# Optimization experiments

Measured on AMD Instinct MI355X. Metric: run time of the kernel, lower is better.

## Reference

```python
import jax, jax.numpy as jnp
import numpy as np

N_NODES = 100000
N_EDGES = 640000
D = 128
L = 3
NUM_GRAPHS = 128


def setup_inputs() -> dict:
    key = jax.random.key(0)
    ks = jax.random.split(key, 8)
    scale = 1.0 / np.sqrt(D)
    x = jax.random.normal(ks[0], (N_NODES, D), dtype=jnp.float32)
    edge_index = jax.random.randint(ks[1], (2, N_EDGES), 0, N_NODES, dtype=jnp.int64)
    batch = jnp.sort(jax.random.randint(ks[2], (N_NODES,), 0, NUM_GRAPHS, dtype=jnp.int64))
    W1 = jax.random.normal(ks[3], (L, D, D), dtype=jnp.float32) * scale
    b1 = jnp.zeros((L, D), dtype=jnp.float32)
    W2 = jax.random.normal(ks[4], (L, D, D), dtype=jnp.float32) * scale
    b2 = jnp.zeros((L, D), dtype=jnp.float32)
    return {"x": x, "edge_index": edge_index, "batch": batch,
            "W1": W1, "b1": b1, "W2": W2, "b2": b2}


def reference(x, edge_index, batch, W1, b1, W2, b2):
    # GIN forward: per layer z = ReLU(MLP((1+eps)*z + sum_{j in N(i)} z_j)), eps=0
    n = x.shape[0]
    src, dst = edge_index[0], edge_index[1]  # messages flow src -> dst
    z = x
    for l in range(W1.shape[0]):
        agg = jax.ops.segment_sum(z[src], dst, num_segments=n)  # scatter-add aggregation
        h = agg + z                                             # (1+eps)*x_i + sum x_j, eps=0
        h = jnp.maximum(h @ W1[l] + b1[l], 0.0)                 # Linear + ReLU
        z = h @ W2[l] + b2[l]                                   # Linear
        z = jnp.maximum(z, 0.0)                                 # F.relu after conv
    # global mean pool over graph ids (dropout is identity in eval / p=0)
    ones = jnp.ones((n,), dtype=z.dtype)
    counts = jax.ops.segment_sum(ones, batch, num_segments=NUM_GRAPHS)
    sums = jax.ops.segment_sum(z, batch, num_segments=NUM_GRAPHS)
    g = sums / jnp.maximum(counts, 1.0)[:, None]
    return z, g
```

## Files before the change

### kernel.cpp

```cpp
#include <hip/hip_runtime.h>
#include <hip/hip_bf16.h>

#define D 128
#define NG 128

typedef __attribute__((ext_vector_type(8))) short bf16x8;
typedef __attribute__((ext_vector_type(4))) float f32x4;

__device__ inline unsigned short f2bf(float f) {
  union { float f; unsigned u; } c; c.f = f;
  unsigned u = c.u;
  return (unsigned short)((u + 0x7FFFu + ((u >> 16) & 1u)) >> 16);
}
__device__ inline float bf2f(unsigned short b) {
  union { unsigned u; float f; } c; c.u = ((unsigned)b) << 16;
  return c.f;
}

__global__ void prep_w(const float* __restrict__ W1, const float* __restrict__ W2,
                       unsigned short* __restrict__ Wt1, unsigned short* __restrict__ Wt2,
                       int* __restrict__ deg, int N, float* __restrict__ g,
                       const int* __restrict__ batch, int* __restrict__ start) {
  int t = blockIdx.x * 256 + threadIdx.x;
  if (t < N) deg[t] = 0;
  if (t < NG * D) g[t] = 0.f;
  if (t < NG) {
    int lo = 0, hi = N;
    while (lo < hi) {
      int mid = (lo + hi) >> 1;
      if (batch[mid] < t) lo = mid + 1; else hi = mid;
    }
    start[t] = lo;
    if (t == 0) start[NG] = N;
  }
  if (t >= 3 * 128 * 128) return;
  int l = t >> 14, k = (t >> 7) & 127, n = t & 127;
  int o = (l << 14) + (n << 7) + k;
  Wt1[o] = f2bf(W1[t]);
  Wt2[o] = f2bf(W2[t]);
}


__global__ void hist_deg(const int* __restrict__ dst, int* __restrict__ deg, int E) {
  int e = blockIdx.x * 256 + threadIdx.x;
  if (e < E) atomicAdd(deg + dst[e], 1);
}

__global__ __launch_bounds__(256) void scan1(const int* __restrict__ deg,
    int* __restrict__ rowptr, int* __restrict__ bsum, int n) {
  __shared__ int sh[256];
  int tid = threadIdx.x;
  int idx = blockIdx.x * 1024 + tid * 4;
  int v[4], tsum = 0;
#pragma unroll
  for (int j = 0; j < 4; ++j) { v[j] = (idx + j < n) ? deg[idx + j] : 0; tsum += v[j]; }
  sh[tid] = tsum;
  __syncthreads();
  for (int off = 1; off < 256; off <<= 1) {
    int x = (tid >= off) ? sh[tid - off] : 0;
    __syncthreads();
    sh[tid] += x;
    __syncthreads();
  }
  if (tid == 255) bsum[blockIdx.x] = sh[255];
  int run = sh[tid] - tsum;
#pragma unroll
  for (int j = 0; j < 4; ++j) { if (idx + j < n) rowptr[idx + j] = run; run += v[j]; }
}

__global__ __launch_bounds__(128) void scan2(int* __restrict__ bsum, int nb) {
  __shared__ int sh[128];
  int tid = threadIdx.x;
  int v = (tid < nb) ? bsum[tid] : 0;
  sh[tid] = v;
  __syncthreads();
  for (int off = 1; off < 128; off <<= 1) {
    int x = (tid >= off) ? sh[tid - off] : 0;
    __syncthreads();
    sh[tid] += x;
    __syncthreads();
  }
  if (tid < nb) bsum[tid] = sh[tid] - v;
}

__global__ void scan3(int* __restrict__ rowptr, int* __restrict__ pos,
                      const int* __restrict__ bsum, int n, int E) {
  int t = blockIdx.x * 256 + threadIdx.x;
  if (t < n) {
    int v = rowptr[t] + bsum[t >> 10];
    rowptr[t] = v;
    pos[t] = v;
  }
  if (t == 0) rowptr[n] = E;
}

__global__ void edge_scatter(const int* __restrict__ src, const int* __restrict__ dst,
                             int* __restrict__ pos, int* __restrict__ csr_src, int E) {
  int e = blockIdx.x * 256 + threadIdx.x;
  if (e >= E) return;
  int idx = atomicAdd(pos + dst[e], 1);
  csr_src[idx] = src[e];
}


template<bool IN_BF16>
__global__ __launch_bounds__(256) void gather_agg(const void* __restrict__ zin,
    const int* __restrict__ rowptr, const int* __restrict__ csr_src,
    unsigned short* __restrict__ agg, int N) {
  int t = blockIdx.x * 256 + threadIdx.x;
  int node = t >> 3;
  if (node >= N) return;
  int c = (t & 7) * 16;
  const float* zf = (const float*)zin;
  const unsigned short* zb = (const unsigned short*)zin;

  float acc[16];

  if constexpr (IN_BF16) {
    const unsigned short* p = zb + (size_t)node * D + c;
    bf16x8 v0 = *(const bf16x8*)(p);
    bf16x8 v1 = *(const bf16x8*)(p + 8);
#pragma unroll
    for (int j = 0; j < 8; ++j) {
      acc[j]     = bf2f((unsigned short)v0[j]);
      acc[j + 8] = bf2f((unsigned short)v1[j]);
    }
  } else {
    const float* p = zf + (size_t)node * D + c;
    float4 v0 = *(const float4*)(p);
    float4 v1 = *(const float4*)(p + 4);
    float4 v2 = *(const float4*)(p + 8);
    float4 v3 = *(const float4*)(p + 12);
    acc[0]  = v0.x; acc[1]  = v0.y; acc[2]  = v0.z; acc[3]  = v0.w;
    acc[4]  = v1.x; acc[5]  = v1.y; acc[6]  = v1.z; acc[7]  = v1.w;
    acc[8]  = v2.x; acc[9]  = v2.y; acc[10] = v2.z; acc[11] = v2.w;
    acc[12] = v3.x; acc[13] = v3.y; acc[14] = v3.z; acc[15] = v3.w;
  }

  int e  = rowptr[node];
  int e1 = rowptr[node + 1];

  if constexpr (IN_BF16) {
    for (; e + 4 <= e1; e += 4) {
      int s0 = csr_src[e + 0];
      int s1 = csr_src[e + 1];
      int s2 = csr_src[e + 2];
      int s3 = csr_src[e + 3];
      const unsigned short* p0 = zb + (size_t)s0 * D + c;
      const unsigned short* p1 = zb + (size_t)s1 * D + c;
      const unsigned short* p2 = zb + (size_t)s2 * D + c;
      const unsigned short* p3 = zb + (size_t)s3 * D + c;
      bf16x8 a0 = *(const bf16x8*)(p0), a1 = *(const bf16x8*)(p0 + 8);
      bf16x8 b0 = *(const bf16x8*)(p1), b1 = *(const bf16x8*)(p1 + 8);
      bf16x8 c0 = *(const bf16x8*)(p2), c1 = *(const bf16x8*)(p2 + 8);
      bf16x8 d0 = *(const bf16x8*)(p3), d1 = *(const bf16x8*)(p3 + 8);
#pragma unroll
      for (int j = 0; j < 8; ++j) {
        acc[j]     += (bf2f((unsigned short)a0[j]) + bf2f((unsigned short)b0[j]))
                    + (bf2f((unsigned short)c0[j]) + bf2f((unsigned short)d0[j]));
        acc[j + 8] += (bf2f((unsigned short)a1[j]) + bf2f((unsigned short)b1[j]))
                    + (bf2f((unsigned short)c1[j]) + bf2f((unsigned short)d1[j]));
      }
    }
    if (e + 2 <= e1) {
      int s0 = csr_src[e + 0];
      int s1 = csr_src[e + 1];
      const unsigned short* p0 = zb + (size_t)s0 * D + c;
      const unsigned short* p1 = zb + (size_t)s1 * D + c;
      bf16x8 a0 = *(const bf16x8*)(p0), a1 = *(const bf16x8*)(p0 + 8);
      bf16x8 b0 = *(const bf16x8*)(p1), b1 = *(const bf16x8*)(p1 + 8);
#pragma unroll
      for (int j = 0; j < 8; ++j) {
        acc[j]     += bf2f((unsigned short)a0[j]) + bf2f((unsigned short)b0[j]);
        acc[j + 8] += bf2f((unsigned short)a1[j]) + bf2f((unsigned short)b1[j]);
      }
      e += 2;
    }
    if (e < e1) {
      int s0 = csr_src[e];
      const unsigned short* p0 = zb + (size_t)s0 * D + c;
      bf16x8 a0 = *(const bf16x8*)(p0), a1 = *(const bf16x8*)(p0 + 8);
#pragma unroll
      for (int j = 0; j < 8; ++j) {
        acc[j]     += bf2f((unsigned short)a0[j]);
        acc[j + 8] += bf2f((unsigned short)a1[j]);
      }
    }
  } else {
    for (; e + 2 <= e1; e += 2) {
      int s0 = csr_src[e + 0];
      int s1 = csr_src[e + 1];
      const float* p0 = zf + (size_t)s0 * D + c;
      const float* p1 = zf + (size_t)s1 * D + c;
      float4 u0 = *(const float4*)(p0);
      float4 u1 = *(const float4*)(p0 + 4);
      float4 u2 = *(const float4*)(p0 + 8);
      float4 u3 = *(const float4*)(p0 + 12);
      float4 w0 = *(const float4*)(p1);
      float4 w1 = *(const float4*)(p1 + 4);
      float4 w2 = *(const float4*)(p1 + 8);
      float4 w3 = *(const float4*)(p1 + 12);
      acc[0]  += u0.x + w0.x; acc[1]  += u0.y + w0.y;
      acc[2]  += u0.z + w0.z; acc[3]  += u0.w + w0.w;
      acc[4]  += u1.x + w1.x; acc[5]  += u1.y + w1.y;
      acc[6]  += u1.z + w1.z; acc[7]  += u1.w + w1.w;
      acc[8]  += u2.x + w2.x; acc[9]  += u2.y + w2.y;
      acc[10] += u2.z + w2.z; acc[11] += u2.w + w2.w;
      acc[12] += u3.x + w3.x; acc[13] += u3.y + w3.y;
      acc[14] += u3.z + w3.z; acc[15] += u3.w + w3.w;
    }
    if (e < e1) {
      int s0 = csr_src[e];
      const float* p0 = zf + (size_t)s0 * D + c;
      float4 u0 = *(const float4*)(p0);
      float4 u1 = *(const float4*)(p0 + 4);
      float4 u2 = *(const float4*)(p0 + 8);
      float4 u3 = *(const float4*)(p0 + 12);
      acc[0]  += u0.x; acc[1]  += u0.y; acc[2]  += u0.z; acc[3]  += u0.w;
      acc[4]  += u1.x; acc[5]  += u1.y; acc[6]  += u1.z; acc[7]  += u1.w;
      acc[8]  += u2.x; acc[9]  += u2.y; acc[10] += u2.z; acc[11] += u2.w;
      acc[12] += u3.x; acc[13] += u3.y; acc[14] += u3.z; acc[15] += u3.w;
    }
  }

  bf16x8 o0, o1;
#pragma unroll
  for (int j = 0; j < 8; ++j) {
    o0[j] = (short)f2bf(acc[j]);
    o1[j] = (short)f2bf(acc[j + 8]);
  }
  unsigned short* q = agg + (size_t)node * D + c;
  *(bf16x8*)(q)     = o0;
  *(bf16x8*)(q + 8) = o1;
}


template<bool LAST>
__global__ __launch_bounds__(256, 2) void gemm_fused(const unsigned short* __restrict__ A,
    const unsigned short* __restrict__ Wt1, const float* __restrict__ b1v,
    const unsigned short* __restrict__ Wt2, const float* __restrict__ b2v,
    unsigned short* __restrict__ Zb, float* __restrict__ Zf, int M, int nt) {
  __shared__ unsigned short w2s[128][136];
  __shared__ unsigned short hs[4][32][136];
  int tid  = threadIdx.x;
  int lane = tid & 63;
  int wid  = tid >> 6;
  int c16  = lane & 15;
  int kq   = lane >> 4;
  int koff = kq * 8;

  int tile0 = blockIdx.x * 2;
  int tile1 = tile0 + 1;

  bf16x8 aA[2][4], aB[2][4];
#pragma unroll
  for (int h = 0; h < 2; ++h) {
    int rowA = tile0 * 128 + wid * 32 + h * 16 + c16;
    rowA = rowA < M ? rowA : M - 1;
    int rowB = tile1 * 128 + wid * 32 + h * 16 + c16;
    rowB = rowB < M ? rowB : M - 1;
#pragma unroll
    for (int kk = 0; kk < 4; ++kk) {
      aA[h][kk] = *(const bf16x8*)(A + (size_t)rowA * D + kk * 32 + koff);
      aB[h][kk] = *(const bf16x8*)(A + (size_t)rowB * D + kk * 32 + koff);
    }
  }

#pragma unroll
  for (int i = 0; i < 8; ++i) {
    int chunk = i * 256 + tid;
    int row = chunk >> 4, k16 = chunk & 15;
    *(bf16x8*)&w2s[row][k16 * 8] = *(const bf16x8*)(Wt2 + (size_t)row * D + k16 * 8);
  }

  bf16x8 bf1[8][4];
  float  bb1[8], bb2[8];
#pragma unroll
  for (int fc = 0; fc < 8; ++fc) {
    int col = fc * 16 + c16;
    bb1[fc] = b1v[col];
    bb2[fc] = b2v[col];
#pragma unroll
    for (int kk = 0; kk < 4; ++kk)
      bf1[fc][kk] = *(const bf16x8*)(Wt1 + (size_t)col * D + kk * 32 + koff);
  }

  __syncthreads();

  auto TILE = [&](const bf16x8 (&a)[2][4], int tile) {
    int rb = tile * 128 + wid * 32;
#pragma unroll
    for (int fc = 0; fc < 8; ++fc) {
      f32x4 acc0 = {0.f, 0.f, 0.f, 0.f};
      f32x4 acc1 = {0.f, 0.f, 0.f, 0.f};
#pragma unroll
      for (int kk = 0; kk < 4; ++kk) {
        acc0 = __builtin_amdgcn_mfma_f32_16x16x32_bf16(a[0][kk], bf1[fc][kk], acc0, 0, 0, 0);
        acc1 = __builtin_amdgcn_mfma_f32_16x16x32_bf16(a[1][kk], bf1[fc][kk], acc1, 0, 0, 0);
      }
      int col = fc * 16 + c16;
#pragma unroll
      for (int r = 0; r < 4; ++r) {
        hs[wid][kq * 4 + r][col]      = f2bf(fmaxf(acc0[r] + bb1[fc], 0.f));
        hs[wid][kq * 4 + r + 16][col] = f2bf(fmaxf(acc1[r] + bb1[fc], 0.f));
      }
    }
    bf16x8 a2[2][4];
#pragma unroll
    for (int fr = 0; fr < 2; ++fr)
#pragma unroll
      for (int kk = 0; kk < 4; ++kk)
        a2[fr][kk] = *(const bf16x8*)&hs[wid][fr * 16 + c16][kk * 32 + koff];
#pragma unroll
    for (int fc = 0; fc < 8; ++fc) {
      f32x4 acc0 = {0.f, 0.f, 0.f, 0.f};
      f32x4 acc1 = {0.f, 0.f, 0.f, 0.f};
      int col = fc * 16 + c16;
#pragma unroll
      for (int kk = 0; kk < 4; ++kk) {
        bf16x8 b = *(const bf16x8*)&w2s[col][kk * 32 + koff];
        acc0 = __builtin_amdgcn_mfma_f32_16x16x32_bf16(a2[0][kk], b, acc0, 0, 0, 0);
        acc1 = __builtin_amdgcn_mfma_f32_16x16x32_bf16(a2[1][kk], b, acc1, 0, 0, 0);
      }
      if constexpr (LAST) {
#pragma unroll
        for (int r = 0; r < 4; ++r) {
          int row0 = rb + kq * 4 + r;
          if (row0 < M) Zf[(size_t)row0 * D + col] = fmaxf(acc0[r] + bb2[fc], 0.f);
          int row1 = row0 + 16;
          if (row1 < M) Zf[(size_t)row1 * D + col] = fmaxf(acc1[r] + bb2[fc], 0.f);
        }
      } else {
#pragma unroll
        for (int r = 0; r < 4; ++r) {
          hs[wid][kq * 4 + r][col]      = f2bf(fmaxf(acc0[r] + bb2[fc], 0.f));
          hs[wid][kq * 4 + r + 16][col] = f2bf(fmaxf(acc1[r] + bb2[fc], 0.f));
        }
      }
    }
    if constexpr (!LAST) {
#pragma unroll
      for (int i = 0; i < 8; ++i) {
        int rl = i * 4 + kq;
        bf16x8 v = *(const bf16x8*)&hs[wid][rl][c16 * 8];
        int row = rb + rl;
        if (row < M)
          *(bf16x8*)(Zb + (size_t)row * D + c16 * 8) = v;
      }
    }
  };

  TILE(aA, tile0);
  if (tile1 < nt) TILE(aB, tile1);
}


#define PCHUNKS 8
__global__ __launch_bounds__(128) void pool_mean(const float* __restrict__ z,
    const int* __restrict__ start, float* __restrict__ g) {
  int gid   = blockIdx.x >> 3;
  int chunk = blockIdx.x & (PCHUNKS - 1);
  int col = threadIdx.x;
  int s = start[gid], epos = start[gid + 1];
  int len = epos - s;
  if (len <= 0) return;
  int per = (len + PCHUNKS - 1) / PCHUNKS;
  int r0 = s + chunk * per;
  int r1 = min(r0 + per, epos);
  if (r0 >= r1) return;
  float a0 = 0.f, a1 = 0.f, a2 = 0.f, a3 = 0.f;
  int i = r0;
  for (; i + 4 <= r1; i += 4) {
    a0 += z[(size_t)(i + 0) * D + col];
    a1 += z[(size_t)(i + 1) * D + col];
    a2 += z[(size_t)(i + 2) * D + col];
    a3 += z[(size_t)(i + 3) * D + col];
  }
  for (; i < r1; ++i) a0 += z[(size_t)i * D + col];
  atomicAdd(g + (size_t)gid * D + col, (a0 + a1) + (a2 + a3));
}

__global__ void pool_div(float* __restrict__ g, const int* __restrict__ start) {
  int t = blockIdx.x * 256 + threadIdx.x;
  if (t >= NG * D) return;
  int gid = t >> 7;
  int cnt = start[gid + 1] - start[gid];
  g[t] = g[t] / fmaxf((float)cnt, 1.f);
}

extern "C" void kernel_launch(void* const* d_in, const int* in_sizes, int n_in,
                              void* d_out, int out_size, void* d_ws, size_t ws_size,
                              hipStream_t stream) {
  const float* x     = (const float*)d_in[0];
  const int*   ei    = (const int*)d_in[1];
  const int*   batch = (const int*)d_in[2];
  const float* W1    = (const float*)d_in[3];
  const float* b1    = (const float*)d_in[4];
  const float* W2    = (const float*)d_in[5];
  const float* b2    = (const float*)d_in[6];

  const int N = in_sizes[0] / D;
  const int E = in_sizes[1] / 2;
  const int* src = ei;
  const int* dst = ei + E;

  float* zout = (float*)d_out;
  float* g    = zout + (size_t)N * D;

  char* w = (char*)d_ws;
  unsigned short* agg     = (unsigned short*)w;    w += (size_t)N * D * 2;
  unsigned short* zb      = (unsigned short*)w;    w += (size_t)N * D * 2;
  unsigned short* Wt1     = (unsigned short*)w;    w += 3 * 16384 * 2;
  unsigned short* Wt2     = (unsigned short*)w;    w += 3 * 16384 * 2;
  int*            start   = (int*)w;               w += (NG + 4) * 4;
  int*            deg     = (int*)w;               w += (size_t)N * 4;
  int*            rowptr  = (int*)w;               w += (size_t)(N + 4) * 4;
  int*            pos     = (int*)w;               w += (size_t)N * 4;
  int*            bsum    = (int*)w;               w += 128 * 4;
  int*            csr_src = (int*)w;               w += (size_t)E * 4;

  const int nb = (N + 1023) / 1024;

  int prep_threads = (3 * 128 * 128 > N) ? 3 * 128 * 128 : N;
  prep_w<<<(prep_threads + 255) / 256, 256, 0, stream>>>(W1, W2, Wt1, Wt2, deg, N, g,
                                                         batch, start);

  hist_deg<<<(E + 255) / 256, 256, 0, stream>>>(dst, deg, E);
  scan1<<<nb, 256, 0, stream>>>(deg, rowptr, bsum, N);
  scan2<<<1, 128, 0, stream>>>(bsum, nb);
  scan3<<<(N + 255) / 256, 256, 0, stream>>>(rowptr, pos, bsum, N, E);
  edge_scatter<<<(E + 255) / 256, 256, 0, stream>>>(src, dst, pos, csr_src, E);

  const int gather_blocks = (int)(((size_t)N * 8 + 255) / 256);
  const int nt            = (N + 127) / 128;
  const int gemm_blocks   = (nt + 1) / 2;

  gather_agg<false><<<gather_blocks, 256, 0, stream>>>(x, rowptr, csr_src, agg, N);
  gemm_fused<false><<<gemm_blocks, 256, 0, stream>>>(agg, Wt1, b1, Wt2, b2, zb, zout, N, nt);
  gather_agg<true><<<gather_blocks, 256, 0, stream>>>(zb, rowptr, csr_src, agg, N);
  gemm_fused<false><<<gemm_blocks, 256, 0, stream>>>(agg, Wt1 + 16384, b1 + 128,
                                                     Wt2 + 16384, b2 + 128, zb, zout, N, nt);
  gather_agg<true><<<gather_blocks, 256, 0, stream>>>(zb, rowptr, csr_src, agg, N);
  gemm_fused<true><<<gemm_blocks, 256, 0, stream>>>(agg, Wt1 + 32768, b1 + 256,
                                                    Wt2 + 32768, b2 + 256, zb, zout, N, nt);

  pool_mean<<<NG * PCHUNKS, 128, 0, stream>>>(zout, start, g);
  pool_div<<<(NG * D + 255) / 256, 256, 0, stream>>>(g, start);
}
```

Before: 279.4 us.

## Fuse CSR build into one cooperative kernel and fold mean division into pooling

Replaces the five CSR construction kernels (degree histogram, three-stage scan, edge scatter) with a single cooperative kernel of 512 blocks that separates phases with grid-wide syncs. Also folds the mean division into pool_mean by scaling partial sums before the atomic add, which removes pool_div. Gather loads of csr_src and stores of agg now use nontemporal hints. Fewer launches cut launch gaps, but the kernel now assumes N ≤ 512*256 and depends on a cooperative launch with grid syncs.

```diff
diff --git a/kernel.cpp b/kernel.cpp
--- a/kernel.cpp
+++ b/kernel.cpp
@@ -1,8 +1,12 @@
 #include <hip/hip_runtime.h>
 #include <hip/hip_bf16.h>
+#include <hip/hip_cooperative_groups.h>
+
+namespace cg = cooperative_groups;
 
 #define D 128
 #define NG 128
+#define CSR_BLOCKS 512
 
 typedef __attribute__((ext_vector_type(8))) short bf16x8;
 typedef __attribute__((ext_vector_type(4))) float f32x4;
@@ -41,20 +45,23 @@
 }
 
 
-__global__ void hist_deg(const int* __restrict__ dst, int* __restrict__ deg, int E) {
-  int e = blockIdx.x * 256 + threadIdx.x;
-  if (e < E) atomicAdd(deg + dst[e], 1);
-}
-
-__global__ __launch_bounds__(256) void scan1(const int* __restrict__ deg,
-    int* __restrict__ rowptr, int* __restrict__ bsum, int n) {
+__global__ __launch_bounds__(256) void csr_build(
+    const int* __restrict__ src, const int* __restrict__ dst,
+    int* __restrict__ deg, int* __restrict__ rowptr, int* __restrict__ pos,
+    int* __restrict__ bsum, int* __restrict__ csr_src, int N, int E) {
+  cg::grid_group grid = cg::this_grid();
   __shared__ int sh[256];
-  int tid = threadIdx.x;
-  int idx = blockIdx.x * 1024 + tid * 4;
-  int v[4], tsum = 0;
-#pragma unroll
-  for (int j = 0; j < 4; ++j) { v[j] = (idx + j < n) ? deg[idx + j] : 0; tsum += v[j]; }
-  sh[tid] = tsum;
+  int tid  = threadIdx.x;
+  int gtid = blockIdx.x * 256 + tid;
+  const int nth = CSR_BLOCKS * 256;
+
+  for (int e = gtid; e < E; e += nth)
+    atomicAdd(deg + dst[e], 1);
+  __threadfence();
+  grid.sync();
+
+  int v = (gtid < N) ? deg[gtid] : 0;
+  sh[tid] = v;
   __syncthreads();
   for (int off = 1; off < 256; off <<= 1) {
     int x = (tid >= off) ? sh[tid - off] : 0;
@@ -63,43 +70,39 @@
     __syncthreads();
   }
   if (tid == 255) bsum[blockIdx.x] = sh[255];
-  int run = sh[tid] - tsum;
-#pragma unroll
-  for (int j = 0; j < 4; ++j) { if (idx + j < n) rowptr[idx + j] = run; run += v[j]; }
-}
-
-__global__ __launch_bounds__(128) void scan2(int* __restrict__ bsum, int nb) {
-  __shared__ int sh[128];
-  int tid = threadIdx.x;
-  int v = (tid < nb) ? bsum[tid] : 0;
-  sh[tid] = v;
-  __syncthreads();
-  for (int off = 1; off < 128; off <<= 1) {
-    int x = (tid >= off) ? sh[tid - off] : 0;
+  int local_ex = sh[tid] - v;
+  __threadfence();
+  grid.sync();
+
+  if (blockIdx.x == 0) {
+    int a = bsum[tid * 2], b = bsum[tid * 2 + 1];
+    int pairsum = a + b;
+    sh[tid] = pairsum;
     __syncthreads();
-    sh[tid] += x;
-    __syncthreads();
-  }
-  if (tid < nb) bsum[tid] = sh[tid] - v;
-}
-
-__global__ void scan3(int* __restrict__ rowptr, int* __restrict__ pos,
-                      const int* __restrict__ bsum, int n, int E) {
-  int t = blockIdx.x * 256 + threadIdx.x;
-  if (t < n) {
-    int v = rowptr[t] + bsum[t >> 10];
-    rowptr[t] = v;
-    pos[t] = v;
-  }
-  if (t == 0) rowptr[n] = E;
-}
-
-__global__ void edge_scatter(const int* __restrict__ src, const int* __restrict__ dst,
-                             int* __restrict__ pos, int* __restrict__ csr_src, int E) {
-  int e = blockIdx.x * 256 + threadIdx.x;
-  if (e >= E) return;
-  int idx = atomicAdd(pos + dst[e], 1);
-  csr_src[idx] = src[e];
+    for (int off = 1; off < 256; off <<= 1) {
+      int x = (tid >= off) ? sh[tid - off] : 0;
+      __syncthreads();
+      sh[tid] += x;
+      __syncthreads();
+    }
+    int ex = sh[tid] - pairsum;
+    bsum[tid * 2]     = ex;
+    bsum[tid * 2 + 1] = ex + a;
+  }
+  __threadfence();
+  grid.sync();
+
+  if (gtid < N) {
+    int val = local_ex + bsum[blockIdx.x];
+    rowptr[gtid] = val;
+    pos[gtid] = val;
+  }
+  if (gtid == 0) rowptr[N] = E;
+  __threadfence();
+  grid.sync();
+
+  for (int e = gtid; e < E; e += nth)
+    csr_src[atomicAdd(pos + dst[e], 1)] = src[e];
 }
 
 
@@ -142,10 +145,10 @@
 
   if constexpr (IN_BF16) {
     for (; e + 4 <= e1; e += 4) {
-      int s0 = csr_src[e + 0];
-      int s1 = csr_src[e + 1];
-      int s2 = csr_src[e + 2];
-      int s3 = csr_src[e + 3];
+      int s0 = __builtin_nontemporal_load(csr_src + e + 0);
+      int s1 = __builtin_nontemporal_load(csr_src + e + 1);
+      int s2 = __builtin_nontemporal_load(csr_src + e + 2);
+      int s3 = __builtin_nontemporal_load(csr_src + e + 3);
       const unsigned short* p0 = zb + (size_t)s0 * D + c;
       const unsigned short* p1 = zb + (size_t)s1 * D + c;
       const unsigned short* p2 = zb + (size_t)s2 * D + c;
@@ -163,8 +166,8 @@
       }
     }
     if (e + 2 <= e1) {
-      int s0 = csr_src[e + 0];
-      int s1 = csr_src[e + 1];
+      int s0 = __builtin_nontemporal_load(csr_src + e + 0);
+      int s1 = __builtin_nontemporal_load(csr_src + e + 1);
       const unsigned short* p0 = zb + (size_t)s0 * D + c;
       const unsigned short* p1 = zb + (size_t)s1 * D + c;
       bf16x8 a0 = *(const bf16x8*)(p0), a1 = *(const bf16x8*)(p0 + 8);
@@ -177,7 +180,7 @@
       e += 2;
     }
     if (e < e1) {
-      int s0 = csr_src[e];
+      int s0 = __builtin_nontemporal_load(csr_src + e);
       const unsigned short* p0 = zb + (size_t)s0 * D + c;
       bf16x8 a0 = *(const bf16x8*)(p0), a1 = *(const bf16x8*)(p0 + 8);
 #pragma unroll
@@ -188,8 +191,8 @@
     }
   } else {
     for (; e + 2 <= e1; e += 2) {
-      int s0 = csr_src[e + 0];
-      int s1 = csr_src[e + 1];
+      int s0 = __builtin_nontemporal_load(csr_src + e + 0);
+      int s1 = __builtin_nontemporal_load(csr_src + e + 1);
       const float* p0 = zf + (size_t)s0 * D + c;
       const float* p1 = zf + (size_t)s1 * D + c;
       float4 u0 = *(const float4*)(p0);
@@ -210,7 +213,7 @@
       acc[14] += u3.z + w3.z; acc[15] += u3.w + w3.w;
     }
     if (e < e1) {
-      int s0 = csr_src[e];
+      int s0 = __builtin_nontemporal_load(csr_src + e);
       const float* p0 = zf + (size_t)s0 * D + c;
       float4 u0 = *(const float4*)(p0);
       float4 u1 = *(const float4*)(p0 + 4);
@@ -230,8 +233,8 @@
     o1[j] = (short)f2bf(acc[j + 8]);
   }
   unsigned short* q = agg + (size_t)node * D + c;
-  *(bf16x8*)(q)     = o0;
-  *(bf16x8*)(q + 8) = o1;
+  __builtin_nontemporal_store(o0, (bf16x8*)(q));
+  __builtin_nontemporal_store(o1, (bf16x8*)(q + 8));
 }
 
 
@@ -364,6 +367,7 @@
   int s = start[gid], epos = start[gid + 1];
   int len = epos - s;
   if (len <= 0) return;
+  float inv = 1.0f / (float)len;
   int per = (len + PCHUNKS - 1) / PCHUNKS;
   int r0 = s + chunk * per;
   int r1 = min(r0 + per, epos);
@@ -377,15 +381,7 @@
     a3 += z[(size_t)(i + 3) * D + col];
   }
   for (; i < r1; ++i) a0 += z[(size_t)i * D + col];
-  atomicAdd(g + (size_t)gid * D + col, (a0 + a1) + (a2 + a3));
-}
-
-__global__ void pool_div(float* __restrict__ g, const int* __restrict__ start) {
-  int t = blockIdx.x * 256 + threadIdx.x;
-  if (t >= NG * D) return;
-  int gid = t >> 7;
-  int cnt = start[gid + 1] - start[gid];
-  g[t] = g[t] / fmaxf((float)cnt, 1.f);
+  atomicAdd(g + (size_t)gid * D + col, ((a0 + a1) + (a2 + a3)) * inv);
 }
 
 extern "C" void kernel_launch(void* const* d_in, const int* in_sizes, int n_in,
@@ -416,20 +412,23 @@
   int*            deg     = (int*)w;               w += (size_t)N * 4;
   int*            rowptr  = (int*)w;               w += (size_t)(N + 4) * 4;
   int*            pos     = (int*)w;               w += (size_t)N * 4;
-  int*            bsum    = (int*)w;               w += 128 * 4;
+  int*            bsum    = (int*)w;               w += CSR_BLOCKS * 4;
   int*            csr_src = (int*)w;               w += (size_t)E * 4;
-
-  const int nb = (N + 1023) / 1024;
 
   int prep_threads = (3 * 128 * 128 > N) ? 3 * 128 * 128 : N;
   prep_w<<<(prep_threads + 255) / 256, 256, 0, stream>>>(W1, W2, Wt1, Wt2, deg, N, g,
                                                          batch, start);
 
-  hist_deg<<<(E + 255) / 256, 256, 0, stream>>>(dst, deg, E);
-  scan1<<<nb, 256, 0, stream>>>(deg, rowptr, bsum, N);
-  scan2<<<1, 128, 0, stream>>>(bsum, nb);
-  scan3<<<(N + 255) / 256, 256, 0, stream>>>(rowptr, pos, bsum, N, E);
-  edge_scatter<<<(E + 255) / 256, 256, 0, stream>>>(src, dst, pos, csr_src, E);
+  {
+    const int* src_ = src;
+    const int* dst_ = dst;
+    int N_ = N, E_ = E;
+    void* args[] = {(void*)&src_, (void*)&dst_, (void*)&deg, (void*)&rowptr,
+                    (void*)&pos, (void*)&bsum, (void*)&csr_src,
+                    (void*)&N_, (void*)&E_};
+    hipLaunchCooperativeKernel((void*)csr_build, dim3(CSR_BLOCKS), dim3(256),
+                               args, 0, stream);
+  }
 
   const int gather_blocks = (int)(((size_t)N * 8 + 255) / 256);
   const int nt            = (N + 127) / 128;
@@ -445,5 +444,4 @@
                                                     Wt2 + 32768, b2 + 256, zb, zout, N, nt);
 
   pool_mean<<<NG * PCHUNKS, 128, 0, stream>>>(zout, start, g);
-  pool_div<<<(NG * D + 255) / 256, 256, 0, stream>>>(g, start);
-}
+}
```

Measured after the change: 643.9 us. 130% more time.
